# Kernel tuning notes

Hardware: AMD Instinct MI355X
Metric: run time of the kernel (lower is better)

Reference implementation:

```python
import jax, jax.numpy as jnp
import numpy as np


def _gather(feat, idx):
    # feat: [B, L, F], idx: [B, L, D] -> [B, L, D, F]  (per-molecule neighbor gather)
    return jax.vmap(lambda f, i: f[i])(feat, idx)


def setup_inputs() -> dict:
    key = jax.random.key(0)
    ks = jax.random.split(key, 16)
    B, L, D, F, FA, FB, R = 256, 128, 6, 200, 39, 10, 2
    s = 0.05
    return {
        "atom_list": jax.random.normal(ks[0], (B, L, FA), jnp.float32),
        "bond_list": jax.random.normal(ks[1], (B, L, FB), jnp.float32),
        "atom_degree": jax.random.randint(ks[2], (B, L, D), 0, L, jnp.int32),
        "bond_degree": jax.random.randint(ks[3], (B, L, D), 0, L, jnp.int32),
        "atom_W": jax.random.normal(ks[4], (F, FA), jnp.float32) * s,
        "atom_b": jax.random.normal(ks[5], (F,), jnp.float32) * s,
        "nbr_W": jax.random.normal(ks[6], (F, FA + FB), jnp.float32) * s,
        "nbr_b": jax.random.normal(ks[7], (F,), jnp.float32) * s,
        "align_W": jax.random.normal(ks[8], (R, 1, 2 * F), jnp.float32) * s,
        "align_b": jax.random.normal(ks[9], (R, 1), jnp.float32) * s,
        "attend_W": jax.random.normal(ks[10], (R, F, F), jnp.float32) * s,
        "attend_b": jax.random.normal(ks[11], (R, F), jnp.float32) * s,
        "gru_Wih": jax.random.normal(ks[12], (R, 3 * F, F), jnp.float32) * s,
        "gru_Whh": jax.random.normal(ks[13], (R, 3 * F, F), jnp.float32) * s,
        "gru_bih": jax.random.normal(ks[14], (R, 3 * F), jnp.float32) * s,
        "gru_bhh": jax.random.normal(ks[15], (R, 3 * F), jnp.float32) * s,
    }


def reference(atom_list, bond_list, atom_degree, bond_degree,
              atom_W, atom_b, nbr_W, nbr_b,
              align_W, align_b, attend_W, attend_b,
              gru_Wih, gru_Whh, gru_bih, gru_bhh):
    B, L, _ = atom_list.shape
    F = atom_W.shape[0]
    R = align_W.shape[0]
    pad = L - 1  # padding atom index convention from metaGAT

    # masks over padded neighbor slots: [B, L, D, 1]
    is_pad = (atom_degree == pad)[..., None]
    attend_mask = jnp.where(is_pad, 0.0, 1.0).astype(atom_list.dtype)
    softmax_mask = jnp.where(is_pad, -9e8, 0.0).astype(atom_list.dtype)

    # initial atom / neighbor embeddings
    atom_feat = jax.nn.leaky_relu(atom_list @ atom_W.T + atom_b)          # [B,L,F]
    atom_nbr = _gather(atom_list, atom_degree)                             # [B,L,D,FA]
    bond_nbr = _gather(bond_list, bond_degree)                             # [B,L,D,FB]
    nbr_feat = jax.nn.leaky_relu(
        jnp.concatenate([atom_nbr, bond_nbr], axis=-1) @ nbr_W.T + nbr_b)  # [B,L,D,F]

    cur = atom_feat  # GRU hidden / query features (activated after first step)
    for d in range(R):
        if d > 0:
            nbr_feat = _gather(cur, atom_degree)  # [B,L,D,F]
        cur_exp = jnp.broadcast_to(cur[:, :, None, :], nbr_feat.shape)
        feat_align = jnp.concatenate([cur_exp, nbr_feat], axis=-1)        # [B,L,D,2F]
        score = jax.nn.leaky_relu(feat_align @ align_W[d].T + align_b[d]) # [B,L,D,1]
        score = score + softmax_mask
        attn = jax.nn.softmax(score, axis=-2) * attend_mask               # [B,L,D,1]
        nbr_t = nbr_feat @ attend_W[d].T + attend_b[d]                    # [B,L,D,F]
        context = jax.nn.elu(jnp.sum(attn * nbr_t, axis=-2))              # [B,L,F]

        # GRUCell(input=context, hidden=cur)
        gi = context @ gru_Wih[d].T + gru_bih[d]                          # [B,L,3F]
        gh = cur @ gru_Whh[d].T + gru_bhh[d]                              # [B,L,3F]
        ir, iz, inn = jnp.split(gi, 3, axis=-1)
        hr, hz, hn = jnp.split(gh, 3, axis=-1)
        r = jax.nn.sigmoid(ir + hr)
        z = jax.nn.sigmoid(iz + hz)
        n = jnp.tanh(inn + r * hn)
        h = (1.0 - z) * n + z * cur
        cur = jax.nn.relu(h)  # activated_features for next step
    return cur
```

## Files before the change

kernel.cpp:

```cpp
#include <hip/hip_runtime.h>

#define B_     256
#define L_     128
#define D_     6
#define F_     200
#define FA_    39
#define FB_    10
#define PAD_   127
#define LMASK  127
#define NT     256
#define KC8    (F_/8)
#define NTILE  16
#define NQ     (NTILE * D_)
#define NF     (B_ * L_ * F_)
#define MSZ    (F_ * F_)
#define NNODES (B_ * L_)
#define NPAIRS (NNODES * D_)
#define KP     224
#define KPP    232
#define KSTEPS 7
#define NTL    13
#define FRAG_TOTAL (14 * NTL * KSTEPS * 64)
#define PN2    32
#define NPREP  (NNODES / PN2)
#define NBF    ((FRAG_TOTAL + NT - 1) / NT)

typedef __attribute__((ext_vector_type(8))) short sh8;
typedef __attribute__((ext_vector_type(4))) float f32x4;

__device__ __forceinline__ float lrelu(float x) { return x >= 0.0f ? x : 0.01f * x; }
__device__ __forceinline__ float sigm(float x)  { return 1.0f / (1.0f + __expf(-x)); }
__device__ __forceinline__ float fast_tanh(float x) {
    const float e = __expf(2.0f * x);
    return 1.0f - 2.0f / (e + 1.0f);
}
__device__ __forceinline__ unsigned short f2b(float x) {
    unsigned int u = __float_as_uint(x);
    unsigned int r = (u + 0x7FFFu + ((u >> 16) & 1u)) >> 16;
    return (unsigned short)r;
}
__device__ __forceinline__ float b2f(unsigned short u) {
    return __uint_as_float(((unsigned int)u) << 16);
}
#define AFRAG(arr, ks) (*(const sh8*)&arr[lane & 15][(ks) * 32 + ((lane >> 4) << 3)])
__device__ __forceinline__ sh8 bfrag(const unsigned short* __restrict__ WFr,
                                     int mat, int t, int ks, int lane) {
    return *(const sh8*)(WFr + ((((size_t)mat * NTL + t) * KSTEPS + ks) * 64 + lane) * 8);
}

__global__ __launch_bounds__(NT)
void prep_frags_kernel(const float* __restrict__ atom_list, const float* __restrict__ bond_list,
                       const float* __restrict__ atom_W, const float* __restrict__ atom_b,
                       const float* __restrict__ nbr_W,
                       const float* __restrict__ attend_W,
                       const float* __restrict__ gru_Wih,
                       const float* __restrict__ gru_Whh,
                       float* __restrict__ cur0, unsigned short* __restrict__ cur0b,
                       unsigned short* __restrict__ PA, unsigned short* __restrict__ PB,
                       unsigned short* __restrict__ WF)
{
    __shared__ float wsh[F_ * (FA_ + FB_)];
    const int tid = threadIdx.x;

    if (blockIdx.x >= NPREP) {
        const int i = (blockIdx.x - NPREP) * NT + tid;
        if (i >= FRAG_TOTAL) return;
        const int lane = i & 63;
        int rest = i >> 6;
        const int ks = rest % KSTEPS; rest /= KSTEPS;
        const int t  = rest % NTL;
        const int m  = rest / NTL;
        const int n  = t * 16 + (lane & 15);
        const int k0 = ks * 32 + ((lane >> 4) << 3);
        const int r = m / 7, tt = m - r * 7;
        const float* src;
        if (tt == 0)      src = attend_W + (size_t)r * MSZ;
        else if (tt <= 3) src = gru_Wih + ((size_t)r * 3 + (tt - 1)) * MSZ;
        else              src = gru_Whh + ((size_t)r * 3 + (tt - 4)) * MSZ;
        unsigned short o[8];
        #pragma unroll
        for (int j = 0; j < 8; ++j) {
            const int k = k0 + j;
            const float v = (n < F_ && k < F_) ? src[(size_t)n * F_ + k] : 0.0f;
            o[j] = f2b(v);
        }
        uint4 w;
        w.x = (unsigned int)o[0] | ((unsigned int)o[1] << 16);
        w.y = (unsigned int)o[2] | ((unsigned int)o[3] << 16);
        w.z = (unsigned int)o[4] | ((unsigned int)o[5] << 16);
        w.w = (unsigned int)o[6] | ((unsigned int)o[7] << 16);
        ((uint4*)WF)[i] = w;
        return;
    }

    const int node0 = blockIdx.x * PN2;
    const int f     = tid;
    const bool valid = (f < F_);
    const int fc    = valid ? f : 0;

    float wa[FA_];
    float wn[FA_ + FB_];

    for (int i = tid; i < F_ * FA_; i += NT) wsh[i] = atom_W[i];
    __syncthreads();
    #pragma unroll
    for (int k = 0; k < FA_; ++k) wa[k] = wsh[fc * FA_ + k];
    __syncthreads();
    for (int i = tid; i < F_ * (FA_ + FB_); i += NT) wsh[i] = nbr_W[i];
    __syncthreads();
    #pragma unroll
    for (int k = 0; k < FA_ + FB_; ++k) wn[k] = wsh[fc * (FA_ + FB_) + k];

    const float ab = atom_b[fc];

    for (int n = 0; n < PN2; ++n) {
        const float* __restrict__ ar = atom_list + (size_t)(node0 + n) * FA_;
        const float* __restrict__ br = bond_list + (size_t)(node0 + n) * FB_;
        float accA = ab, accPA = 0.0f, accPB = 0.0f;
        #pragma unroll
        for (int k = 0; k < FA_; ++k) {
            const float a = ar[k];
            accA  += a * wa[k];
            accPA += a * wn[k];
        }
        #pragma unroll
        for (int k = 0; k < FB_; ++k) accPB += br[k] * wn[FA_ + k];
        if (valid) {
            const size_t o = (size_t)(node0 + n) * F_ + f;
            const float c = lrelu(accA);
            cur0[o]  = c;
            cur0b[o] = f2b(c);
            PA[o]    = f2b(accPA);
            PB[o]    = f2b(accPB);
        }
    }
}

#define PPB 32
__global__ __launch_bounds__(NT)
void pair_score_kernel(const int* __restrict__ atom_degree,
                       const int* __restrict__ bond_degree,
                       const unsigned short* __restrict__ PA,
                       const unsigned short* __restrict__ PB,
                       const float* __restrict__ alW2, const float* __restrict__ nbr_b,
                       float* __restrict__ s2p)
{
    __shared__ float w_s[F_], b_s[F_];
    const int tid = threadIdx.x;
    if (tid < F_) { w_s[tid] = alW2[tid]; b_s[tid] = nbr_b[tid]; }
    const int xcd = blockIdx.x & 7;
    const int j   = blockIdx.x >> 3;
    const int mol = (j / 24) * 8 + xcd;
    const int q0  = mol * (L_ * D_) + (j % 24) * PPB;
    const int q   = q0 + (tid >> 3);
    const int sub = tid & 7;
    const int nidx = atom_degree[q] & LMASK;
    const int bidx = bond_degree[q] & LMASK;
    const int bL   = mol * L_;
    const unsigned short* pa = PA + (size_t)(bL + nidx) * F_;
    const unsigned short* pb = PB + (size_t)(bL + bidx) * F_;
    __syncthreads();
    float s = 0.0f;
    for (int kk = sub; kk < KC8; kk += 8) {
        const sh8 pa8 = *(const sh8*)(pa + kk * 8);
        const sh8 pb8 = *(const sh8*)(pb + kk * 8);
        #pragma unroll
        for (int e = 0; e < 8; ++e)
            s += lrelu(b2f((unsigned short)pa8[e]) + b2f((unsigned short)pb8[e])
                       + b_s[kk * 8 + e]) * w_s[kk * 8 + e];
    }
    s += __shfl_xor(s, 1, 8); s += __shfl_xor(s, 2, 8); s += __shfl_xor(s, 4, 8);
    if (sub == 0) s2p[q] = s;
}

__global__ __launch_bounds__(NT, 4)
void round_kernel(
    const int*   __restrict__ atom_degree,
    const int*   __restrict__ bond_degree,
    const float* __restrict__ align_W,
    const float* __restrict__ align_b,
    const unsigned short* __restrict__ WF,
    const float* __restrict__ attend_b,
    const float* __restrict__ gru_bih,
    const float* __restrict__ gru_bhh,
    const float* __restrict__ nbr_b,
    const unsigned short* __restrict__ PAb,
    const unsigned short* __restrict__ PBb,
    const float* __restrict__ s2_tab,
    const float* __restrict__ cur_in,
    const unsigned short* __restrict__ cur_inb,
    float*       __restrict__ dst,
    unsigned short* __restrict__ dstb,
    const float* __restrict__ alW2_next,
    float*       __restrict__ s2_next,
    int mode)
{
    const int bid   = blockIdx.x;
    const int mol   = ((bid >> 6) << 3) | (bid & 7);
    const int tile  = (bid >> 3) & 7;
    const int node0 = mol * L_ + tile * NTILE;
    const int bL    = mol * L_;
    const int tid   = threadIdx.x;
    const int lane  = tid & 63;
    const int wave  = tid >> 6;

    __shared__ __align__(16) unsigned short curb  [NTILE][KPP];
    __shared__ __align__(16) unsigned short mixedb[NTILE][KPP];
    __shared__ __align__(16) unsigned short ctxb  [NTILE][KPP];
    __shared__ __align__(16) float nbrb_s[F_];
    __shared__ float sc_s [NQ];
    __shared__ float asum_s[NTILE];
    __shared__ float s1_s[NTILE];
    __shared__ float s2acc[NTILE];
    __shared__ int   nidx_s[NQ];
    __shared__ int   bidx_s[NQ];

    for (int idx = tid; idx < NTILE * (KP - F_); idx += NT) {
        const int n = idx / (KP - F_), k = F_ + idx % (KP - F_);
        curb[n][k] = 0; mixedb[n][k] = 0; ctxb[n][k] = 0;
    }
    if (tid < NTILE) s2acc[tid] = 0.0f;

    if (tid < NQ) {
        const int n = tid / D_, j = tid - n * D_;
        nidx_s[tid] = atom_degree[(node0 + n) * D_ + j] & LMASK;
        bidx_s[tid] = (mode == 0) ? (bond_degree[(node0 + n) * D_ + j] & LMASK) : 0;
    }
    if (mode == 0 && tid < F_) nbrb_s[tid] = nbr_b[tid];

    for (int idx = tid; idx < NTILE * KC8; idx += NT) {
        const int n = idx / KC8, kk = idx - n * KC8;
        *(uint4*)&curb[n][kk * 8] =
            *(const uint4*)(cur_inb + (size_t)(node0 + n) * F_ + kk * 8);
    }

    {
        const int n = tid >> 4, sub = tid & 15;
        const float* crow = cur_in + (size_t)(node0 + n) * F_;
        float a = 0.0f;
        for (int f = sub; f < F_; f += 16) a += crow[f] * align_W[f];
        a += __shfl_xor(a, 1, 16); a += __shfl_xor(a, 2, 16);
        a += __shfl_xor(a, 4, 16); a += __shfl_xor(a, 8, 16);
        if (sub == 0) s1_s[n] = a;
    }
    __syncthreads();

    if (tid < NQ) {
        const int n = tid / D_;
        const float s2v = (mode == 0)
            ? s2_tab[(size_t)(node0 + n) * D_ + (tid - n * D_)]
            : s2_tab[bL + nidx_s[tid]];
        float sc = lrelu(s1_s[n] + s2v + align_b[0]);
        if (nidx_s[tid] == PAD_) sc += -9.0e8f;
        sc_s[tid] = sc;
    }
    __syncthreads();

    if (tid < NTILE) {
        float m = sc_s[tid * D_];
        #pragma unroll
        for (int j = 1; j < D_; ++j) m = fmaxf(m, sc_s[tid * D_ + j]);
        float ex[D_]; float ssum = 0.0f;
        #pragma unroll
        for (int j = 0; j < D_; ++j) { ex[j] = __expf(sc_s[tid * D_ + j] - m); ssum += ex[j]; }
        const float inv = 1.0f / ssum;
        float as = 0.0f;
        #pragma unroll
        for (int j = 0; j < D_; ++j) {
            const float a = (nidx_s[tid * D_ + j] == PAD_) ? 0.0f : ex[j] * inv;
            sc_s[tid * D_ + j] = a;
            as += a;
        }
        asum_s[tid] = as;
    }
    __syncthreads();

    for (int idx = tid; idx < NTILE * KC8; idx += NT) {
        const int n = idx / KC8, kk = idx - n * KC8;
        const int c0 = kk * 8;
        float m[8];
        #pragma unroll
        for (int e = 0; e < 8; ++e) m[e] = 0.0f;
        if (mode == 0) {
            #pragma unroll
            for (int j = 0; j < D_; ++j) {
                const float a = sc_s[n * D_ + j];
                const sh8 pa8 = *(const sh8*)(PAb + (size_t)(bL + nidx_s[n*D_+j]) * F_ + c0);
                const sh8 pb8 = *(const sh8*)(PBb + (size_t)(bL + bidx_s[n*D_+j]) * F_ + c0);
                #pragma unroll
                for (int e = 0; e < 8; ++e)
                    m[e] += a * lrelu(b2f((unsigned short)pa8[e])
                                    + b2f((unsigned short)pb8[e]) + nbrb_s[c0 + e]);
            }
        } else {
            #pragma unroll
            for (int j = 0; j < D_; ++j) {
                const float a = sc_s[n * D_ + j];
                const sh8 v8 = *(const sh8*)(cur_inb + (size_t)(bL + nidx_s[n*D_+j]) * F_ + c0);
                #pragma unroll
                for (int e = 0; e < 8; ++e)
                    m[e] += a * b2f((unsigned short)v8[e]);
            }
        }
        uint4 w;
        w.x = (unsigned int)f2b(m[0]) | ((unsigned int)f2b(m[1]) << 16);
        w.y = (unsigned int)f2b(m[2]) | ((unsigned int)f2b(m[3]) << 16);
        w.z = (unsigned int)f2b(m[4]) | ((unsigned int)f2b(m[5]) << 16);
        w.w = (unsigned int)f2b(m[6]) | ((unsigned int)f2b(m[7]) << 16);
        *(uint4*)&mixedb[n][c0] = w;
    }
    __syncthreads();

    for (int t = wave; t < NTL; t += 4) {
        f32x4 acc = {0.f, 0.f, 0.f, 0.f};
        #pragma unroll
        for (int ks = 0; ks < KSTEPS; ++ks)
            acc = __builtin_amdgcn_mfma_f32_16x16x32_bf16(
                AFRAG(mixedb, ks), bfrag(WF, 0, t, ks, lane), acc, 0, 0, 0);
        const int f = t * 16 + (lane & 15);
        if (f < F_) {
            const float bb = attend_b[f];
            #pragma unroll
            for (int rg = 0; rg < 4; ++rg) {
                const int node = ((lane >> 4) << 2) + rg;
                float c = acc[rg] + asum_s[node] * bb;
                c = (c > 0.0f) ? c : (__expf(c) - 1.0f);
                ctxb[node][f] = f2b(c);
            }
        }
    }
    __syncthreads();

    float s2part[4] = {0.f, 0.f, 0.f, 0.f};
    for (int t = wave; t < NTL; t += 4) {
        f32x4 ar = {0.f,0.f,0.f,0.f}, az = {0.f,0.f,0.f,0.f};
        f32x4 ani = {0.f,0.f,0.f,0.f}, anh = {0.f,0.f,0.f,0.f};
        #pragma unroll
        for (int ks = 0; ks < KSTEPS; ++ks) {
            const sh8 ac = AFRAG(ctxb, ks);
            const sh8 ah = AFRAG(curb, ks);
            ar  = __builtin_amdgcn_mfma_f32_16x16x32_bf16(ac, bfrag(WF,1,t,ks,lane), ar, 0,0,0);
            ar  = __builtin_amdgcn_mfma_f32_16x16x32_bf16(ah, bfrag(WF,4,t,ks,lane), ar, 0,0,0);
            az  = __builtin_amdgcn_mfma_f32_16x16x32_bf16(ac, bfrag(WF,2,t,ks,lane), az, 0,0,0);
            az  = __builtin_amdgcn_mfma_f32_16x16x32_bf16(ah, bfrag(WF,5,t,ks,lane), az, 0,0,0);
            ani = __builtin_amdgcn_mfma_f32_16x16x32_bf16(ac, bfrag(WF,3,t,ks,lane), ani, 0,0,0);
            anh = __builtin_amdgcn_mfma_f32_16x16x32_bf16(ah, bfrag(WF,6,t,ks,lane), anh, 0,0,0);
        }
        const int f = t * 16 + (lane & 15);
        if (f < F_) {
            const float bir = gru_bih[f],        bhr = gru_bhh[f];
            const float biz = gru_bih[F_ + f],   bhz = gru_bhh[F_ + f];
            const float bin = gru_bih[2*F_ + f], bhn = gru_bhh[2*F_ + f];
            const float w2 = (mode == 0) ? alW2_next[f] : 0.0f;
            #pragma unroll
            for (int rg = 0; rg < 4; ++rg) {
                const int node = ((lane >> 4) << 2) + rg;
                const float r  = sigm(ar[rg] + bir + bhr);
                const float z  = sigm(az[rg] + biz + bhz);
                const float nn = fast_tanh(ani[rg] + bin + r * (anh[rg] + bhn));
                const size_t o = (size_t)(node0 + node) * F_ + f;
                const float cv = cur_in[o];
                const float h  = fmaxf((1.0f - z) * nn + z * cv, 0.0f);
                dst[o] = h;
                if (mode == 0) { dstb[o] = f2b(h); s2part[rg] += h * w2; }
            }
        }
    }

    if (mode == 0) {
        #pragma unroll
        for (int rg = 0; rg < 4; ++rg) {
            float v = s2part[rg];
            v += __shfl_xor(v, 1, 16); v += __shfl_xor(v, 2, 16);
            v += __shfl_xor(v, 4, 16); v += __shfl_xor(v, 8, 16);
            if ((lane & 15) == 0) atomicAdd(&s2acc[((lane >> 4) << 2) + rg], v);
        }
        __syncthreads();
        if (tid < NTILE) s2_next[node0 + tid] = s2acc[tid];
    }
}

extern "C" __attribute__((visibility("default")))
void kernel_launch(void* const* d_in, const int* in_sizes, int n_in,
                   void* d_out, int out_size, void* d_ws, size_t ws_size,
                   hipStream_t stream) {
    const float* atom_list = (const float*)d_in[0];
    const float* bond_list = (const float*)d_in[1];
    const int*   atom_deg  = (const int*)d_in[2];
    const int*   bond_deg  = (const int*)d_in[3];
    const float* atom_W    = (const float*)d_in[4];
    const float* atom_b    = (const float*)d_in[5];
    const float* nbr_W     = (const float*)d_in[6];
    const float* nbr_b     = (const float*)d_in[7];
    const float* align_W   = (const float*)d_in[8];
    const float* align_b   = (const float*)d_in[9];
    const float* attend_W  = (const float*)d_in[10];
    const float* attend_b  = (const float*)d_in[11];
    const float* gru_Wih   = (const float*)d_in[12];
    const float* gru_Whh   = (const float*)d_in[13];
    const float* gru_bih   = (const float*)d_in[14];
    const float* gru_bhh   = (const float*)d_in[15];

    float* ws   = (float*)d_ws;
    float* cur0 = ws;
    float* cur1 = ws + (size_t)NF;
    float* s2b  = ws + (size_t)2*NF;
    float* s2p  = s2b + NNODES;
    unsigned short* cur0b = (unsigned short*)(s2p + NPAIRS);
    unsigned short* cur1b = cur0b + (size_t)NF;
    unsigned short* PAb   = cur1b + (size_t)NF;
    unsigned short* PBb   = PAb   + (size_t)NF;
    unsigned short* WF    = PBb   + (size_t)NF;
    float* out  = (float*)d_out;

    prep_frags_kernel<<<dim3(NPREP + NBF), dim3(NT), 0, stream>>>(
        atom_list, bond_list, atom_W, atom_b, nbr_W,
        attend_W, gru_Wih, gru_Whh,
        cur0, cur0b, PAb, PBb, WF);

    pair_score_kernel<<<dim3(NPAIRS / PPB), dim3(NT), 0, stream>>>(
        atom_deg, bond_deg, PAb, PBb, align_W + F_, nbr_b, s2p);

    const dim3 grid(NNODES / NTILE);
    const size_t rframe = (size_t)7 * NTL * KSTEPS * 64 * 8;

    round_kernel<<<grid, dim3(NT), 0, stream>>>(
        atom_deg, bond_deg, align_W, align_b,
        WF, attend_b, gru_bih, gru_bhh,
        nbr_b, PAb, PBb, s2p, cur0, cur0b, cur1, cur1b,
        align_W + 2 * F_ + F_, s2b, 0);

    round_kernel<<<grid, dim3(NT), 0, stream>>>(
        atom_deg, bond_deg, align_W + 2 * F_, align_b + 1,
        WF + rframe, attend_b + F_, gru_bih + 3 * F_, gru_bhh + 3 * F_,
        nbr_b, PAb, PBb, s2b, cur1, cur1b, out, nullptr,
        nullptr, nullptr, 1);
}
```

Baseline: 350.7 us.

## Stage prep inputs in LDS and fuse attention softmax into warp shuffles

After: 340.1 us. 3.0% less time.

```diff
diff --git a/kernel.cpp b/kernel.cpp
--- a/kernel.cpp
+++ b/kernel.cpp
@@ -110,12 +110,21 @@
     __syncthreads();
     #pragma unroll
     for (int k = 0; k < FA_ + FB_; ++k) wn[k] = wsh[fc * (FA_ + FB_) + k];
+    __syncthreads();
+
+    {
+        const float* asrc = atom_list + (size_t)node0 * FA_;
+        for (int i = tid; i < PN2 * FA_; i += NT) wsh[i] = asrc[i];
+        const float* bsrc = bond_list + (size_t)node0 * FB_;
+        for (int i = tid; i < PN2 * FB_; i += NT) wsh[PN2 * FA_ + i] = bsrc[i];
+    }
+    __syncthreads();
 
     const float ab = atom_b[fc];
 
     for (int n = 0; n < PN2; ++n) {
-        const float* __restrict__ ar = atom_list + (size_t)(node0 + n) * FA_;
-        const float* __restrict__ br = bond_list + (size_t)(node0 + n) * FB_;
+        const float* __restrict__ ar = &wsh[n * FA_];
+        const float* __restrict__ br = &wsh[PN2 * FA_ + n * FB_];
         float accA = ab, accPA = 0.0f, accPB = 0.0f;
         #pragma unroll
         for (int k = 0; k < FA_; ++k) {
@@ -210,7 +219,6 @@
     __shared__ __align__(16) float nbrb_s[F_];
     __shared__ float sc_s [NQ];
     __shared__ float asum_s[NTILE];
-    __shared__ float s1_s[NTILE];
     __shared__ float s2acc[NTILE];
     __shared__ int   nidx_s[NQ];
     __shared__ int   bidx_s[NQ];
@@ -220,12 +228,6 @@
         curb[n][k] = 0; mixedb[n][k] = 0; ctxb[n][k] = 0;
     }
     if (tid < NTILE) s2acc[tid] = 0.0f;
-
-    if (tid < NQ) {
-        const int n = tid / D_, j = tid - n * D_;
-        nidx_s[tid] = atom_degree[(node0 + n) * D_ + j] & LMASK;
-        bidx_s[tid] = (mode == 0) ? (bond_degree[(node0 + n) * D_ + j] & LMASK) : 0;
-    }
     if (mode == 0 && tid < F_) nbrb_s[tid] = nbr_b[tid];
 
     for (int idx = tid; idx < NTILE * KC8; idx += NT) {
@@ -237,41 +239,42 @@
     {
         const int n = tid >> 4, sub = tid & 15;
         const float* crow = cur_in + (size_t)(node0 + n) * F_;
-        float a = 0.0f;
-        for (int f = sub; f < F_; f += 16) a += crow[f] * align_W[f];
-        a += __shfl_xor(a, 1, 16); a += __shfl_xor(a, 2, 16);
-        a += __shfl_xor(a, 4, 16); a += __shfl_xor(a, 8, 16);
-        if (sub == 0) s1_s[n] = a;
-    }
-    __syncthreads();
-
-    if (tid < NQ) {
-        const int n = tid / D_;
-        const float s2v = (mode == 0)
-            ? s2_tab[(size_t)(node0 + n) * D_ + (tid - n * D_)]
-            : s2_tab[bL + nidx_s[tid]];
-        float sc = lrelu(s1_s[n] + s2v + align_b[0]);
-        if (nidx_s[tid] == PAD_) sc += -9.0e8f;
-        sc_s[tid] = sc;
-    }
-    __syncthreads();
-
-    if (tid < NTILE) {
-        float m = sc_s[tid * D_];
-        #pragma unroll
-        for (int j = 1; j < D_; ++j) m = fmaxf(m, sc_s[tid * D_ + j]);
-        float ex[D_]; float ssum = 0.0f;
-        #pragma unroll
-        for (int j = 0; j < D_; ++j) { ex[j] = __expf(sc_s[tid * D_ + j] - m); ssum += ex[j]; }
+        float s1 = 0.0f;
+        for (int f = sub; f < F_; f += 16) s1 += crow[f] * align_W[f];
+        s1 += __shfl_xor(s1, 1, 16); s1 += __shfl_xor(s1, 2, 16);
+        s1 += __shfl_xor(s1, 4, 16); s1 += __shfl_xor(s1, 8, 16);
+        float sc = -3.0e38f;
+        int nidx = 0, bidx = 0;
+        if (sub < D_) {
+            nidx = atom_degree[(node0 + n) * D_ + sub] & LMASK;
+            if (mode == 0) bidx = bond_degree[(node0 + n) * D_ + sub] & LMASK;
+            const float s2v = (mode == 0)
+                ? s2_tab[(size_t)(node0 + n) * D_ + sub]
+                : s2_tab[bL + nidx];
+            sc = lrelu(s1 + s2v + align_b[0]);
+            if (nidx == PAD_) sc += -9.0e8f;
+        }
+        float mx = sc;
+        mx = fmaxf(mx, __shfl_xor(mx, 1, 8));
+        mx = fmaxf(mx, __shfl_xor(mx, 2, 8));
+        mx = fmaxf(mx, __shfl_xor(mx, 4, 8));
+        const float ex = __expf(sc - mx);
+        float ssum = ex;
+        ssum += __shfl_xor(ssum, 1, 8);
+        ssum += __shfl_xor(ssum, 2, 8);
+        ssum += __shfl_xor(ssum, 4, 8);
         const float inv = 1.0f / ssum;
-        float as = 0.0f;
-        #pragma unroll
-        for (int j = 0; j < D_; ++j) {
-            const float a = (nidx_s[tid * D_ + j] == PAD_) ? 0.0f : ex[j] * inv;
-            sc_s[tid * D_ + j] = a;
-            as += a;
-        }
-        asum_s[tid] = as;
+        const float aw = (sub < D_ && nidx != PAD_) ? ex * inv : 0.0f;
+        if (sub < D_) {
+            sc_s[n * D_ + sub]   = aw;
+            nidx_s[n * D_ + sub] = nidx;
+            if (mode == 0) bidx_s[n * D_ + sub] = bidx;
+        }
+        float as = aw;
+        as += __shfl_xor(as, 1, 8);
+        as += __shfl_xor(as, 2, 8);
+        as += __shfl_xor(as, 4, 8);
+        if (sub == 0) asum_s[n] = as;
     }
     __syncthreads();
 
```
